# Kernel tuning notes

Hardware: AMD Instinct MI355X
Metric: run time of the kernel (lower is better)

## Reference

```python
import jax, jax.numpy as jnp
import numpy as np

EPS = 1e-10


def setup_inputs() -> dict:
    key = jax.random.key(0)
    k1, k2, k3 = jax.random.split(key, 3)
    B, X, Y = 16, 512, 512
    predictions = jax.random.uniform(k1, (B, 5, X, Y), dtype=jnp.float32)
    inputs = jax.random.uniform(k2, (B, 3, X, Y), dtype=jnp.float32)
    heart = jax.random.randint(k3, (B, 1, X, Y), 0, 2, dtype=jnp.int32)
    return {"predictions": predictions, "inputs": inputs, "heart": heart}


def reference(predictions, inputs, heart):
    # predictions: [B,5,X,Y] soft class maps (chan 0 unused); inputs: [B,3,X,Y] MRI modalities
    # heart: [B,1,X,Y] binary ROI mask. Loops over b/k/m in the torch source are vectorized;
    # boolean-mask gathers become multiply-by-mask with masked reductions (same math).
    mask = (heart[:, 0] == 1).astype(predictions.dtype)          # [B,X,Y]
    pred = predictions[:, 1:5]                                   # [B,K=4,X,Y]
    inp = inputs                                                 # [B,M=3,X,Y]

    w = pred * mask[:, None]                                     # masked soft weights [B,K,X,Y]
    sw = jnp.sum(w, axis=(2, 3))                                 # [B,K]
    denom = sw[:, :, None] + EPS                                 # [B,K,1]

    # per-(k,m) weighted mean over masked pixels
    mu = jnp.einsum('bkxy,bmxy->bkm', w, inp) / denom            # [B,K,M]
    diff = inp[:, None, :, :, :] - mu[:, :, :, None, None]       # [B,K,M,X,Y]
    var = jnp.einsum('bkxy,bkmxy->bkm', w, diff * diff) / denom + EPS

    # Gaussian pdf per (k,m,pixel), scaled by pred_k (as in temp[k,m] = pred[k]*pdf)
    inv_norm = 1.0 / jnp.sqrt(2.0 * jnp.pi * var)                # [B,K,M]
    pdf = inv_norm[:, :, :, None, None] * jnp.exp(
        -(diff * diff) / (2.0 * var)[:, :, :, None, None])      # [B,K,M,X,Y]
    temp = pred[:, :, None] * pdf                                # [B,K,M,X,Y]

    mix = jnp.sum(jnp.prod(temp, axis=2), axis=1)                # [B,X,Y]
    loglik = jnp.log(mix + EPS)                                  # [B,X,Y]

    # masked mean over ROI pixels per batch (== torch.mean over gathered pixels)
    per_b = -jnp.sum(loglik * mask, axis=(1, 2)) / jnp.sum(mask, axis=(1, 2))
    return jnp.mean(per_b)
```

## Files before the change

kernel.cpp:

```cpp
#include <hip/hip_runtime.h>
#include <math.h>

constexpr int NB = 16;
constexpr int XY = 512 * 512;
constexpr int NV = XY / 4;

constexpr int G1 = 128;
constexpr int NIT1 = NV / (G1 * 64);
constexpr int G2 = 64;
constexpr int NIT2 = NV / (G2 * 256);

constexpr int P1OFF = 4096;
constexpr int P2OFF = P1OFF + NB * G1 * 32 * 4;

__device__ __forceinline__ float waveReduce64(float v) {
#pragma unroll
    for (int off = 32; off > 0; off >>= 1) v += __shfl_down(v, off, 64);
    return v;
}

__device__ __forceinline__ float rfl(float x) {
    return __uint_as_float(__builtin_amdgcn_readfirstlane(__float_as_uint(x)));
}

#define PIXW(h_, p_, e0_, e1_, e2_) do {                                      \
    float mm_ = ((h_) == 1) ? 1.f : 0.f;                                      \
    cnt += mm_;                                                               \
    float w_ = (p_) * mm_;                                                    \
    s0 += w_;                                                                 \
    float t_;                                                                 \
    t_ = w_ * (e0_); u0 += t_; q0 = fmaf(t_, (e0_), q0);                      \
    t_ = w_ * (e1_); u1 += t_; q1 = fmaf(t_, (e1_), q1);                      \
    t_ = w_ * (e2_); u2 += t_; q2 = fmaf(t_, (e2_), q2);                      \
} while (0)

#define PARAMK(K_, mu0_, mu1_, mu2_, h0_, h1_, h2_, C_) {                     \
    double S0_ = tot[1 + (K_)];                                               \
    double den_ = S0_ + 1e-10;                                                \
    double Cd_ = 1.0;                                                         \
    double S1_, S2_, muv_, var_;                                              \
    S1_ = tot[5 + (K_)*3 + 0]; S2_ = tot[17 + (K_)*3 + 0];                    \
    muv_ = S1_ / den_;                                                        \
    var_ = (S2_ - 2.0 * muv_ * S1_ + muv_ * muv_ * S0_) / den_ + 1e-10;       \
    mu0_ = (float)muv_; h0_ = (float)(0.5 / var_);                            \
    Cd_ *= 1.0 / sqrt(6.283185307179586 * var_);                              \
    S1_ = tot[5 + (K_)*3 + 1]; S2_ = tot[17 + (K_)*3 + 1];                    \
    muv_ = S1_ / den_;                                                        \
    var_ = (S2_ - 2.0 * muv_ * S1_ + muv_ * muv_ * S0_) / den_ + 1e-10;       \
    mu1_ = (float)muv_; h1_ = (float)(0.5 / var_);                            \
    Cd_ *= 1.0 / sqrt(6.283185307179586 * var_);                              \
    S1_ = tot[5 + (K_)*3 + 2]; S2_ = tot[17 + (K_)*3 + 2];                    \
    muv_ = S1_ / den_;                                                        \
    var_ = (S2_ - 2.0 * muv_ * S1_ + muv_ * muv_ * S0_) / den_ + 1e-10;       \
    mu2_ = (float)muv_; h2_ = (float)(0.5 / var_);                            \
    Cd_ *= 1.0 / sqrt(6.283185307179586 * var_);                              \
    C_ = (float)Cd_;                                                          \
}

#define PIX2(h_, e0_, e1_, e2_, p0_, p1_, p2_, p3_) do {                      \
    float m_ = ((h_) == 1) ? 1.f : 0.f;                                       \
    float d0_, d1_, d2_, ex_, pc_;                                            \
    float mix_;                                                               \
    d0_ = (e0_) - mu00; d1_ = (e1_) - mu01; d2_ = (e2_) - mu02;               \
    ex_ = fmaf(d0_ * d0_, hv00, fmaf(d1_ * d1_, hv01, d2_ * d2_ * hv02));     \
    pc_ = (p0_) * (p0_) * (p0_);                                              \
    mix_ = C0 * pc_ * __expf(-ex_);                                           \
    d0_ = (e0_) - mu10; d1_ = (e1_) - mu11; d2_ = (e2_) - mu12;               \
    ex_ = fmaf(d0_ * d0_, hv10, fmaf(d1_ * d1_, hv11, d2_ * d2_ * hv12));     \
    pc_ = (p1_) * (p1_) * (p1_);                                              \
    mix_ = fmaf(C1 * pc_, __expf(-ex_), mix_);                                \
    d0_ = (e0_) - mu20; d1_ = (e1_) - mu21; d2_ = (e2_) - mu22;               \
    ex_ = fmaf(d0_ * d0_, hv20, fmaf(d1_ * d1_, hv21, d2_ * d2_ * hv22));     \
    pc_ = (p2_) * (p2_) * (p2_);                                              \
    mix_ = fmaf(C2 * pc_, __expf(-ex_), mix_);                                \
    d0_ = (e0_) - mu30; d1_ = (e1_) - mu31; d2_ = (e2_) - mu32;               \
    ex_ = fmaf(d0_ * d0_, hv30, fmaf(d1_ * d1_, hv31, d2_ * d2_ * hv32));     \
    pc_ = (p3_) * (p3_) * (p3_);                                              \
    mix_ = fmaf(C3 * pc_, __expf(-ex_), mix_);                                \
    lacc += m_ * __logf(mix_ + 1e-10f);                                       \
} while (0)

__global__ __launch_bounds__(256) void pass1_moments(
        const float* __restrict__ predictions,
        const float* __restrict__ inputs,
        const int*   __restrict__ heart,
        char*        __restrict__ wsraw) {
    const int b    = blockIdx.y;
    const int g    = blockIdx.x;
    const int tid  = threadIdx.x;
    const int lane = tid & 63;
    const int wav  = tid >> 6;

    const float4* PK = reinterpret_cast<const float4*>(
        predictions + (size_t)b * 5 * XY + (size_t)(1 + wav) * XY);
    const float4* I0 = reinterpret_cast<const float4*>(inputs + (size_t)b * 3 * XY + 0 * XY);
    const float4* I1 = reinterpret_cast<const float4*>(inputs + (size_t)b * 3 * XY + 1 * XY);
    const float4* I2 = reinterpret_cast<const float4*>(inputs + (size_t)b * 3 * XY + 2 * XY);
    const int4*   H  = reinterpret_cast<const int4*>(heart + (size_t)b * XY);

    float cnt = 0.f, s0 = 0.f;
    float u0 = 0.f, u1 = 0.f, u2 = 0.f;
    float q0 = 0.f, q1 = 0.f, q2 = 0.f;

#pragma unroll 4
    for (int it = 0; it < NIT1; ++it) {
        const int v = g * 64 + lane + it * (G1 * 64);
        int4   h  = H[v];
        float4 pk = PK[v];
        float4 f0 = I0[v], f1 = I1[v], f2 = I2[v];
        PIXW(h.x, pk.x, f0.x, f1.x, f2.x);
        PIXW(h.y, pk.y, f0.y, f1.y, f2.y);
        PIXW(h.z, pk.z, f0.z, f1.z, f2.z);
        PIXW(h.w, pk.w, f0.w, f1.w, f2.w);
    }

    s0 = waveReduce64(s0);
    u0 = waveReduce64(u0); u1 = waveReduce64(u1); u2 = waveReduce64(u2);
    q0 = waveReduce64(q0); q1 = waveReduce64(q1); q2 = waveReduce64(q2);
    if (wav == 0) cnt = waveReduce64(cnt);

    if (lane == 0) {
        float* dst = reinterpret_cast<float*>(wsraw + P1OFF) + (((size_t)b * G1 + g) << 5);
        dst[1 + wav]           = s0;
        dst[5 + 3 * wav + 0]   = u0;
        dst[5 + 3 * wav + 1]   = u1;
        dst[5 + 3 * wav + 2]   = u2;
        dst[17 + 3 * wav + 0]  = q0;
        dst[17 + 3 * wav + 1]  = q1;
        dst[17 + 3 * wav + 2]  = q2;
        if (wav == 0) dst[0]   = cnt;
    }
}

__global__ __launch_bounds__(256) void reduce_totals(char* __restrict__ wsraw) {
    const int b   = blockIdx.x;
    const int tid = threadIdx.x;
    const float* p1 = reinterpret_cast<const float*>(wsraw + P1OFF) + ((size_t)b * G1 << 5);
    __shared__ double red[8][32];
    const int col = tid & 31, r = tid >> 5;
    double s = 0.0;
    if (col < 29) {
#pragma unroll
        for (int j = r; j < G1; j += 8) s += (double)p1[((size_t)j << 5) + col];
    }
    red[r][col] = s;
    __syncthreads();
    if (tid < 29) {
        double t = 0.0;
#pragma unroll
        for (int r2 = 0; r2 < 8; ++r2) t += red[r2][tid];
        reinterpret_cast<double*>(wsraw)[(size_t)b * 32 + tid] = t;
    }
}

__global__ __launch_bounds__(256) void pass2_loglik(
        const float* __restrict__ predictions,
        const float* __restrict__ inputs,
        const int*   __restrict__ heart,
        char*        __restrict__ wsraw) {
    const int b   = blockIdx.y;
    const int g   = blockIdx.x;
    const int tid = threadIdx.x;
    const double* tot = reinterpret_cast<const double*>(wsraw) + (size_t)b * 32;

    float mu00, mu01, mu02, mu10, mu11, mu12, mu20, mu21, mu22, mu30, mu31, mu32;
    float hv00, hv01, hv02, hv10, hv11, hv12, hv20, hv21, hv22, hv30, hv31, hv32;
    float C0, C1, C2, C3;
    PARAMK(0, mu00, mu01, mu02, hv00, hv01, hv02, C0);
    PARAMK(1, mu10, mu11, mu12, hv10, hv11, hv12, C1);
    PARAMK(2, mu20, mu21, mu22, hv20, hv21, hv22, C2);
    PARAMK(3, mu30, mu31, mu32, hv30, hv31, hv32, C3);
    mu00=rfl(mu00); mu01=rfl(mu01); mu02=rfl(mu02);
    mu10=rfl(mu10); mu11=rfl(mu11); mu12=rfl(mu12);
    mu20=rfl(mu20); mu21=rfl(mu21); mu22=rfl(mu22);
    mu30=rfl(mu30); mu31=rfl(mu31); mu32=rfl(mu32);
    hv00=rfl(hv00); hv01=rfl(hv01); hv02=rfl(hv02);
    hv10=rfl(hv10); hv11=rfl(hv11); hv12=rfl(hv12);
    hv20=rfl(hv20); hv21=rfl(hv21); hv22=rfl(hv22);
    hv30=rfl(hv30); hv31=rfl(hv31); hv32=rfl(hv32);
    C0=rfl(C0); C1=rfl(C1); C2=rfl(C2); C3=rfl(C3);

    const float4* P1 = reinterpret_cast<const float4*>(predictions + (size_t)b * 5 * XY + 1 * XY);
    const float4* P2 = reinterpret_cast<const float4*>(predictions + (size_t)b * 5 * XY + 2 * XY);
    const float4* P3 = reinterpret_cast<const float4*>(predictions + (size_t)b * 5 * XY + 3 * XY);
    const float4* P4 = reinterpret_cast<const float4*>(predictions + (size_t)b * 5 * XY + 4 * XY);
    const float4* I0 = reinterpret_cast<const float4*>(inputs + (size_t)b * 3 * XY + 0 * XY);
    const float4* I1 = reinterpret_cast<const float4*>(inputs + (size_t)b * 3 * XY + 1 * XY);
    const float4* I2 = reinterpret_cast<const float4*>(inputs + (size_t)b * 3 * XY + 2 * XY);
    const int4*   H  = reinterpret_cast<const int4*>(heart + (size_t)b * XY);

    float lacc = 0.f;
#pragma unroll 2
    for (int it = 0; it < NIT2; ++it) {
        const int v = g * 256 + tid + it * (G2 * 256);
        int4   h  = H[v];
        float4 f0 = I0[v], f1 = I1[v], f2 = I2[v];
        float4 g0 = P1[v], g1 = P2[v], g2 = P3[v], g3 = P4[v];
        PIX2(h.x, f0.x, f1.x, f2.x, g0.x, g1.x, g2.x, g3.x);
        PIX2(h.y, f0.y, f1.y, f2.y, g0.y, g1.y, g2.y, g3.y);
        PIX2(h.z, f0.z, f1.z, f2.z, g0.z, g1.z, g2.z, g3.z);
        PIX2(h.w, f0.w, f1.w, f2.w, g0.w, g1.w, g2.w, g3.w);
    }

    __shared__ float sh2[4];
    const int lane = tid & 63;
    const int wav  = tid >> 6;
    {
        float v = waveReduce64(lacc);
        if (lane == 0) sh2[wav] = v;
    }
    __syncthreads();
    if (tid == 0) {
        float* p2 = reinterpret_cast<float*>(wsraw + P2OFF);
        p2[(size_t)b * G2 + g] = sh2[0] + sh2[1] + sh2[2] + sh2[3];
    }
}

__global__ __launch_bounds__(256) void finalize_kernel(
        const char* __restrict__ wsraw, float* __restrict__ out) {
    const float*  p2  = reinterpret_cast<const float*>(wsraw + P2OFF);
    const double* tot = reinterpret_cast<const double*>(wsraw);
    __shared__ double red[16][17];
    const int tid = threadIdx.x;
    const int b = tid >> 4, r = tid & 15;
    double s = 0.0;
#pragma unroll
    for (int j = r; j < G2; j += 16)
        s += (double)p2[(size_t)b * G2 + j];
    red[b][r] = s;
    __syncthreads();
    double v = 0.0;
    if (tid < NB) {
        double l = 0.0;
#pragma unroll
        for (int r2 = 0; r2 < 16; ++r2) l += red[tid][r2];
        v = -l / tot[(size_t)tid * 32];
    }
#pragma unroll
    for (int off = 8; off > 0; off >>= 1) v += __shfl_down(v, off, 64);
    if (tid == 0) out[0] = (float)(v / (double)NB);
}

extern "C" void kernel_launch(void* const* d_in, const int* in_sizes, int n_in,
                              void* d_out, int out_size, void* d_ws, size_t ws_size,
                              hipStream_t stream) {
    const float* predictions = (const float*)d_in[0];
    const float* inputs      = (const float*)d_in[1];
    const int*   heart       = (const int*)d_in[2];
    float* out   = (float*)d_out;
    char*  wsraw = (char*)d_ws;

    pass1_moments<<<dim3(G1, NB), 256, 0, stream>>>(predictions, inputs, heart, wsraw);
    reduce_totals<<<dim3(NB),     256, 0, stream>>>(wsraw);
    pass2_loglik <<<dim3(G2, NB), 256, 0, stream>>>(predictions, inputs, heart, wsraw);
    finalize_kernel<<<1,          256, 0, stream>>>(wsraw, out);
}
```

Baseline: 195.0 us.

## Stage tiles into LDS with async global_load_lds double-buffering in both passes

Both passes now stream the 8 input planes into double-buffered shared memory using the direct global-to-LDS load builtin, prefetching the next window while the current one is computed. Pass1 is restructured so every thread accumulates moments for all four classes instead of one wave per class, with a block-level LDS reduction. Grid sizes drop to 32 blocks per batch for both passes. The goal is to hide memory latency and keep more loads in flight per CU on a bandwidth-bound workload. The cost is more registers per thread, 64KB of LDS per block (lower occupancy), and fewer blocks overall.

```diff
diff --git a/kernel.cpp b/kernel.cpp
--- a/kernel.cpp
+++ b/kernel.cpp
@@ -1,14 +1,16 @@
 #include <hip/hip_runtime.h>
 #include <math.h>
-
-constexpr int NB = 16;
-constexpr int XY = 512 * 512;
-constexpr int NV = XY / 4;
-
-constexpr int G1 = 128;
-constexpr int NIT1 = NV / (G1 * 64);
-constexpr int G2 = 64;
-constexpr int NIT2 = NV / (G2 * 256);
+#include <stdint.h>
+
+constexpr int NB  = 16;
+constexpr int XY  = 512 * 512;
+constexpr int NV  = XY / 4;
+
+constexpr int G1  = 32;
+constexpr int WIN = 256;
+constexpr int NIT = NV / (G1 * WIN);
+constexpr int NPL = 8;
+static_assert((NIT & 1) == 0, "LDS-reuse epilogue assumes last window lives in buf1");
 
 constexpr int P1OFF = 4096;
 constexpr int P2OFF = P1OFF + NB * G1 * 32 * 4;
@@ -23,15 +25,32 @@
     return __uint_as_float(__builtin_amdgcn_readfirstlane(__float_as_uint(x)));
 }
 
-#define PIXW(h_, p_, e0_, e1_, e2_) do {                                      \
+__device__ __forceinline__ void gl2lds(const void* g, void* l) {
+    __builtin_amdgcn_global_load_lds(
+        (__attribute__((address_space(1))) void*)(void*)g,
+        (__attribute__((address_space(3))) void*)l,
+        16, 0, 0);
+}
+
+#define PIX1(h_, e0_, e1_, e2_, p0_, p1_, p2_, p3_) do {                      \
     float mm_ = ((h_) == 1) ? 1.f : 0.f;                                      \
     cnt += mm_;                                                               \
-    float w_ = (p_) * mm_;                                                    \
-    s0 += w_;                                                                 \
+    float w0_ = (p0_) * mm_, w1_ = (p1_) * mm_, w2_ = (p2_) * mm_,            \
+          w3_ = (p3_) * mm_;                                                  \
+    s0_0 += w0_; s0_1 += w1_; s0_2 += w2_; s0_3 += w3_;                       \
     float t_;                                                                 \
-    t_ = w_ * (e0_); u0 += t_; q0 = fmaf(t_, (e0_), q0);                      \
-    t_ = w_ * (e1_); u1 += t_; q1 = fmaf(t_, (e1_), q1);                      \
-    t_ = w_ * (e2_); u2 += t_; q2 = fmaf(t_, (e2_), q2);                      \
+    t_ = w0_ * (e0_); u00 += t_; q00 = fmaf(t_, (e0_), q00);                  \
+    t_ = w0_ * (e1_); u01 += t_; q01 = fmaf(t_, (e1_), q01);                  \
+    t_ = w0_ * (e2_); u02 += t_; q02 = fmaf(t_, (e2_), q02);                  \
+    t_ = w1_ * (e0_); u10 += t_; q10 = fmaf(t_, (e0_), q10);                  \
+    t_ = w1_ * (e1_); u11 += t_; q11 = fmaf(t_, (e1_), q11);                  \
+    t_ = w1_ * (e2_); u12 += t_; q12 = fmaf(t_, (e2_), q12);                  \
+    t_ = w2_ * (e0_); u20 += t_; q20 = fmaf(t_, (e0_), q20);                  \
+    t_ = w2_ * (e1_); u21 += t_; q21 = fmaf(t_, (e1_), q21);                  \
+    t_ = w2_ * (e2_); u22 += t_; q22 = fmaf(t_, (e2_), q22);                  \
+    t_ = w3_ * (e0_); u30 += t_; q30 = fmaf(t_, (e0_), q30);                  \
+    t_ = w3_ * (e1_); u31 += t_; q31 = fmaf(t_, (e1_), q31);                  \
+    t_ = w3_ * (e2_); u32 += t_; q32 = fmaf(t_, (e2_), q32);                  \
 } while (0)
 
 #define PARAMK(K_, mu0_, mu1_, mu2_, h0_, h1_, h2_, C_) {                     \
@@ -80,6 +99,47 @@
     lacc += m_ * __logf(mix_ + 1e-10f);                                       \
 } while (0)
 
+#define STAGE(B_, IT_) do {                                                   \
+    const size_t o_ = (size_t)(IT_) * 4096;                                   \
+    char* lb_ = lds + (B_) * (NPL * 4096) + wav * 1024;                       \
+    gl2lds(gH  + o_, lb_ + 0 * 4096);                                         \
+    gl2lds(gI0 + o_, lb_ + 1 * 4096);                                         \
+    gl2lds(gI1 + o_, lb_ + 2 * 4096);                                         \
+    gl2lds(gI2 + o_, lb_ + 3 * 4096);                                         \
+    gl2lds(gP1 + o_, lb_ + 4 * 4096);                                         \
+    gl2lds(gP2 + o_, lb_ + 5 * 4096);                                         \
+    gl2lds(gP3 + o_, lb_ + 6 * 4096);                                         \
+    gl2lds(gP4 + o_, lb_ + 7 * 4096);                                         \
+} while (0)
+
+#define LOADREGS(B_)                                                          \
+    const char* cb_ = lds + (B_) * (NPL * 4096);                              \
+    int4   h  = *(const int4*)  (cb_ + 0 * 4096 + tid * 16);                  \
+    float4 f0 = *(const float4*)(cb_ + 1 * 4096 + tid * 16);                  \
+    float4 f1 = *(const float4*)(cb_ + 2 * 4096 + tid * 16);                  \
+    float4 f2 = *(const float4*)(cb_ + 3 * 4096 + tid * 16);                  \
+    float4 g0 = *(const float4*)(cb_ + 4 * 4096 + tid * 16);                  \
+    float4 g1 = *(const float4*)(cb_ + 5 * 4096 + tid * 16);                  \
+    float4 g2 = *(const float4*)(cb_ + 6 * 4096 + tid * 16);                  \
+    float4 g3 = *(const float4*)(cb_ + 7 * 4096 + tid * 16);
+
+#define DECL_GSRC                                                             \
+    const char* Pb = (const char*)(predictions + (size_t)b * 5 * XY);         \
+    const char* Ib = (const char*)(inputs      + (size_t)b * 3 * XY);         \
+    const char* Hb = (const char*)(heart       + (size_t)b * XY);             \
+    const size_t vb = (size_t)(g * (NIT * WIN) + wav * 64 + lane) * 16;       \
+    const char* gH  = Hb + vb;                                                \
+    const char* gI0 = Ib + 0 * (size_t)XY * 4 + vb;                           \
+    const char* gI1 = Ib + 1 * (size_t)XY * 4 + vb;                           \
+    const char* gI2 = Ib + 2 * (size_t)XY * 4 + vb;                           \
+    const char* gP1 = Pb + 1 * (size_t)XY * 4 + vb;                           \
+    const char* gP2 = Pb + 2 * (size_t)XY * 4 + vb;                           \
+    const char* gP3 = Pb + 3 * (size_t)XY * 4 + vb;                           \
+    const char* gP4 = Pb + 4 * (size_t)XY * 4 + vb;
+
+#define WAIT_LGKM  asm volatile("s_waitcnt lgkmcnt(0)" ::: "memory")
+#define WAIT_VM    asm volatile("s_waitcnt vmcnt(0)"   ::: "memory")
+
 __global__ __launch_bounds__(256) void pass1_moments(
         const float* __restrict__ predictions,
         const float* __restrict__ inputs,
@@ -91,44 +151,49 @@
     const int lane = tid & 63;
     const int wav  = tid >> 6;
 
-    const float4* PK = reinterpret_cast<const float4*>(
-        predictions + (size_t)b * 5 * XY + (size_t)(1 + wav) * XY);
-    const float4* I0 = reinterpret_cast<const float4*>(inputs + (size_t)b * 3 * XY + 0 * XY);
-    const float4* I1 = reinterpret_cast<const float4*>(inputs + (size_t)b * 3 * XY + 1 * XY);
-    const float4* I2 = reinterpret_cast<const float4*>(inputs + (size_t)b * 3 * XY + 2 * XY);
-    const int4*   H  = reinterpret_cast<const int4*>(heart + (size_t)b * XY);
-
-    float cnt = 0.f, s0 = 0.f;
-    float u0 = 0.f, u1 = 0.f, u2 = 0.f;
-    float q0 = 0.f, q1 = 0.f, q2 = 0.f;
-
-#pragma unroll 4
-    for (int it = 0; it < NIT1; ++it) {
-        const int v = g * 64 + lane + it * (G1 * 64);
-        int4   h  = H[v];
-        float4 pk = PK[v];
-        float4 f0 = I0[v], f1 = I1[v], f2 = I2[v];
-        PIXW(h.x, pk.x, f0.x, f1.x, f2.x);
-        PIXW(h.y, pk.y, f0.y, f1.y, f2.y);
-        PIXW(h.z, pk.z, f0.z, f1.z, f2.z);
-        PIXW(h.w, pk.w, f0.w, f1.w, f2.w);
-    }
-
-    s0 = waveReduce64(s0);
-    u0 = waveReduce64(u0); u1 = waveReduce64(u1); u2 = waveReduce64(u2);
-    q0 = waveReduce64(q0); q1 = waveReduce64(q1); q2 = waveReduce64(q2);
-    if (wav == 0) cnt = waveReduce64(cnt);
-
-    if (lane == 0) {
-        float* dst = reinterpret_cast<float*>(wsraw + P1OFF) + (((size_t)b * G1 + g) << 5);
-        dst[1 + wav]           = s0;
-        dst[5 + 3 * wav + 0]   = u0;
-        dst[5 + 3 * wav + 1]   = u1;
-        dst[5 + 3 * wav + 2]   = u2;
-        dst[17 + 3 * wav + 0]  = q0;
-        dst[17 + 3 * wav + 1]  = q1;
-        dst[17 + 3 * wav + 2]  = q2;
-        if (wav == 0) dst[0]   = cnt;
+    __shared__ __align__(16) char lds[2 * NPL * 4096];
+
+    DECL_GSRC;
+
+    float cnt = 0.f;
+    float s0_0 = 0.f, s0_1 = 0.f, s0_2 = 0.f, s0_3 = 0.f;
+    float u00 = 0.f, u01 = 0.f, u02 = 0.f, u10 = 0.f, u11 = 0.f, u12 = 0.f;
+    float u20 = 0.f, u21 = 0.f, u22 = 0.f, u30 = 0.f, u31 = 0.f, u32 = 0.f;
+    float q00 = 0.f, q01 = 0.f, q02 = 0.f, q10 = 0.f, q11 = 0.f, q12 = 0.f;
+    float q20 = 0.f, q21 = 0.f, q22 = 0.f, q30 = 0.f, q31 = 0.f, q32 = 0.f;
+
+    STAGE(0, 0);
+    WAIT_VM;
+    for (int it = 0; it < NIT; ++it) {
+        LOADREGS(it & 1);
+        WAIT_LGKM;
+        if (it + 1 < NIT) STAGE((it + 1) & 1, it + 1);
+        PIX1(h.x, f0.x, f1.x, f2.x, g0.x, g1.x, g2.x, g3.x);
+        PIX1(h.y, f0.y, f1.y, f2.y, g0.y, g1.y, g2.y, g3.y);
+        PIX1(h.z, f0.z, f1.z, f2.z, g0.z, g1.z, g2.z, g3.z);
+        PIX1(h.w, f0.w, f1.w, f2.w, g0.w, g1.w, g2.w, g3.w);
+        WAIT_VM;
+    }
+
+    __syncthreads();
+    float* shred = reinterpret_cast<float*>(lds);
+#define REDS(i_, var_) { float r_ = waveReduce64(var_); if (lane == 0) shred[wav * 32 + (i_)] = r_; }
+    REDS(0, cnt);
+    REDS(1, s0_0); REDS(2, s0_1); REDS(3, s0_2); REDS(4, s0_3);
+    REDS(5, u00); REDS(6, u01); REDS(7, u02);
+    REDS(8, u10); REDS(9, u11); REDS(10, u12);
+    REDS(11, u20); REDS(12, u21); REDS(13, u22);
+    REDS(14, u30); REDS(15, u31); REDS(16, u32);
+    REDS(17, q00); REDS(18, q01); REDS(19, q02);
+    REDS(20, q10); REDS(21, q11); REDS(22, q12);
+    REDS(23, q20); REDS(24, q21); REDS(25, q22);
+    REDS(26, q30); REDS(27, q31); REDS(28, q32);
+#undef REDS
+    __syncthreads();
+    if (tid < 29) {
+        float v = shred[tid] + shred[32 + tid] + shred[64 + tid] + shred[96 + tid];
+        float* p1 = reinterpret_cast<float*>(wsraw + P1OFF);
+        p1[(((size_t)b * G1 + g) << 5) + tid] = v;
     }
 }
 
@@ -158,9 +223,14 @@
         const float* __restrict__ inputs,
         const int*   __restrict__ heart,
         char*        __restrict__ wsraw) {
-    const int b   = blockIdx.y;
-    const int g   = blockIdx.x;
-    const int tid = threadIdx.x;
+    const int b    = blockIdx.y;
+    const int g    = blockIdx.x;
+    const int tid  = threadIdx.x;
+    const int lane = tid & 63;
+    const int wav  = tid >> 6;
+
+    __shared__ __align__(16) char lds[2 * NPL * 4096];
+
     const double* tot = reinterpret_cast<const double*>(wsraw) + (size_t)b * 32;
 
     float mu00, mu01, mu02, mu10, mu11, mu12, mu20, mu21, mu22, mu30, mu31, mu32;
@@ -180,39 +250,33 @@
     hv30=rfl(hv30); hv31=rfl(hv31); hv32=rfl(hv32);
     C0=rfl(C0); C1=rfl(C1); C2=rfl(C2); C3=rfl(C3);
 
-    const float4* P1 = reinterpret_cast<const float4*>(predictions + (size_t)b * 5 * XY + 1 * XY);
-    const float4* P2 = reinterpret_cast<const float4*>(predictions + (size_t)b * 5 * XY + 2 * XY);
-    const float4* P3 = reinterpret_cast<const float4*>(predictions + (size_t)b * 5 * XY + 3 * XY);
-    const float4* P4 = reinterpret_cast<const float4*>(predictions + (size_t)b * 5 * XY + 4 * XY);
-    const float4* I0 = reinterpret_cast<const float4*>(inputs + (size_t)b * 3 * XY + 0 * XY);
-    const float4* I1 = reinterpret_cast<const float4*>(inputs + (size_t)b * 3 * XY + 1 * XY);
-    const float4* I2 = reinterpret_cast<const float4*>(inputs + (size_t)b * 3 * XY + 2 * XY);
-    const int4*   H  = reinterpret_cast<const int4*>(heart + (size_t)b * XY);
+    DECL_GSRC;
 
     float lacc = 0.f;
-#pragma unroll 2
-    for (int it = 0; it < NIT2; ++it) {
-        const int v = g * 256 + tid + it * (G2 * 256);
-        int4   h  = H[v];
-        float4 f0 = I0[v], f1 = I1[v], f2 = I2[v];
-        float4 g0 = P1[v], g1 = P2[v], g2 = P3[v], g3 = P4[v];
+
+    STAGE(0, 0);
+    WAIT_VM;
+    for (int it = 0; it < NIT; ++it) {
+        LOADREGS(it & 1);
+        WAIT_LGKM;
+        if (it + 1 < NIT) STAGE((it + 1) & 1, it + 1);
         PIX2(h.x, f0.x, f1.x, f2.x, g0.x, g1.x, g2.x, g3.x);
         PIX2(h.y, f0.y, f1.y, f2.y, g0.y, g1.y, g2.y, g3.y);
         PIX2(h.z, f0.z, f1.z, f2.z, g0.z, g1.z, g2.z, g3.z);
         PIX2(h.w, f0.w, f1.w, f2.w, g0.w, g1.w, g2.w, g3.w);
-    }
-
-    __shared__ float sh2[4];
-    const int lane = tid & 63;
-    const int wav  = tid >> 6;
+        WAIT_VM;
+    }
+
+    __syncthreads();
+    float* shred = reinterpret_cast<float*>(lds);
     {
         float v = waveReduce64(lacc);
-        if (lane == 0) sh2[wav] = v;
+        if (lane == 0) shred[wav] = v;
     }
     __syncthreads();
     if (tid == 0) {
         float* p2 = reinterpret_cast<float*>(wsraw + P2OFF);
-        p2[(size_t)b * G2 + g] = sh2[0] + sh2[1] + sh2[2] + sh2[3];
+        p2[(size_t)b * G1 + g] = shred[0] + shred[1] + shred[2] + shred[3];
     }
 }
 
@@ -225,8 +289,8 @@
     const int b = tid >> 4, r = tid & 15;
     double s = 0.0;
 #pragma unroll
-    for (int j = r; j < G2; j += 16)
-        s += (double)p2[(size_t)b * G2 + j];
+    for (int j = r; j < G1; j += 16)
+        s += (double)p2[(size_t)b * G1 + j];
     red[b][r] = s;
     __syncthreads();
     double v = 0.0;
@@ -252,6 +316,6 @@
 
     pass1_moments<<<dim3(G1, NB), 256, 0, stream>>>(predictions, inputs, heart, wsraw);
     reduce_totals<<<dim3(NB),     256, 0, stream>>>(wsraw);
-    pass2_loglik <<<dim3(G2, NB), 256, 0, stream>>>(predictions, inputs, heart, wsraw);
+    pass2_loglik <<<dim3(G1, NB), 256, 0, stream>>>(predictions, inputs, heart, wsraw);
     finalize_kernel<<<1,          256, 0, stream>>>(wsraw, out);
 }
```

Measured after the change: 194.8 us. About the same (-0.1%).
